# Optimization experiments

Hardware: AMD Instinct MI355X
Metric: run time of the kernel (lower is better)

Reference implementation:

```python
import jax, jax.numpy as jnp
import numpy as np


def _chamfer_min_sqdist(a, b):
    # a: [N,3], b: [M,3] -> for each point in a, min squared distance to b. [N]
    # ||a||^2 + ||b||^2 - 2 a.b^T ; clamp tiny negatives from cancellation.
    a2 = jnp.sum(a * a, axis=-1)            # [N]
    b2 = jnp.sum(b * b, axis=-1)            # [M]
    cross = a @ b.T                          # [N,M] GEMM, K=3
    d = a2[:, None] + b2[None, :] - 2.0 * cross
    return jnp.maximum(jnp.min(d, axis=1), 0.0)


def setup_inputs() -> dict:
    key = jax.random.key(0)
    k1, k2 = jax.random.split(key)
    N = 16384
    state_x = jax.random.normal(k1, (N, 3), dtype=jnp.float32)
    target = jax.random.normal(k2, (N, 3), dtype=jnp.float32)
    return {"state_x": state_x, "target": target}


def reference(state_x, target):
    # dist1: target -> nearest in state_x ; dist2: state_x -> nearest in target
    dist1 = _chamfer_min_sqdist(target, state_x)   # [N]
    dist2 = _chamfer_min_sqdist(state_x, target)   # [N]
    loss = (jnp.mean(jnp.sqrt(dist1)) + jnp.mean(jnp.sqrt(dist2))) * 0.5
    return loss * 10.0
```

## Files before the change

kernel.cpp:

```cpp
#include <hip/hip_runtime.h>
#include <math.h>


typedef __attribute__((ext_vector_type(8)))  short bf16x8;
typedef __attribute__((ext_vector_type(16))) float f32x16;

#define S_SLICES 8

__device__ __forceinline__ unsigned enc_f32(float f) {
    int b = __float_as_int(f);
    return (b >= 0) ? ((unsigned)b | 0x80000000u) : ~(unsigned)b;
}
__device__ __forceinline__ float dec_f32(unsigned k) {
    int b = (k & 0x80000000u) ? (int)(k & 0x7FFFFFFFu) : ~(int)k;
    return __int_as_float(b);
}

__device__ __forceinline__ unsigned short f2bf(float v) {
    unsigned u = __float_as_uint(v);
    u += 0x7FFFu + ((u >> 16) & 1u);
    return (unsigned short)(u >> 16);
}
__device__ __forceinline__ float bf2f(unsigned short b) {
    unsigned u = ((unsigned)b) << 16;
    return __uint_as_float(u);
}
__device__ __forceinline__ unsigned pk2(unsigned short lo, unsigned short hi) {
    return (unsigned)lo | ((unsigned)hi << 16);
}

__global__ __launch_bounds__(256) void chamfer_prep(
    const float* __restrict__ state_x, const float* __restrict__ target,
    uint4* __restrict__ AfragS, uint4* __restrict__ AfragT,
    uint4* __restrict__ BfragS, uint4* __restrict__ BfragT,
    unsigned* __restrict__ mins_u, float* __restrict__ out, int N)
{
    const int p = blockIdx.x * 256 + threadIdx.x;
    const float* src = (p < N) ? state_x : target;
    const int i = (p < N) ? p : p - N;

    const float x = src[3*i+0], y = src[3*i+1], z = src[3*i+2];
    const float n2 = fmaf(x, x, fmaf(y, y, z * z));

    const unsigned short hx = f2bf(x), hy = f2bf(y), hz = f2bf(z);
    const unsigned short lx = f2bf(x - bf2f(hx));
    const unsigned short ly = f2bf(y - bf2f(hy));
    const unsigned short lz = f2bf(z - bf2f(hz));
    const unsigned short mhx = f2bf(-2.0f*x), mhy = f2bf(-2.0f*y), mhz = f2bf(-2.0f*z);
    const unsigned short mlx = f2bf(-2.0f*x - bf2f(mhx));
    const unsigned short mly = f2bf(-2.0f*y - bf2f(mhy));
    const unsigned short mlz = f2bf(-2.0f*z - bf2f(mhz));
    const unsigned short hn = f2bf(n2);
    const unsigned short ln = f2bf(n2 - bf2f(hn));
    const unsigned short ONE = 0x3F80;

    uint4 A0 = make_uint4(pk2(mhx,mhy), pk2(mhz,mlx), pk2(mly,mlz), pk2(mhx,mhy));
    uint4 A1 = make_uint4(pk2(mhz,mlx), pk2(mly,mlz), pk2(hn,ln),   pk2(ONE,ONE));
    uint4 B0 = make_uint4(pk2(hx,hy), pk2(hz,hx), pk2(hy,hz), pk2(lx,ly));
    uint4 B1 = make_uint4(pk2(lz,lx), pk2(ly,lz), pk2(ONE,ONE), pk2(hn,ln));

    uint4* Aarr = (p < N) ? AfragS : AfragT;
    uint4* Barr = (p < N) ? BfragS : BfragT;
    Aarr[2*i+0] = A0;  Aarr[2*i+1] = A1;
    Barr[2*i+0] = B0;  Barr[2*i+1] = B1;

    mins_u[p] = 0xFFFFFFFFu;
    if (p == 0) *out = 0.0f;
}

__global__ __launch_bounds__(256) void chamfer_main(
    const bf16x8* __restrict__ AfragS, const bf16x8* __restrict__ AfragT,
    const bf16x8* __restrict__ BfragS, const bf16x8* __restrict__ BfragT,
    unsigned* __restrict__ mins_u, int N, int S)
{
    const int tid  = threadIdx.x;
    const int lane = tid & 63;
    const int l31  = lane & 31;
    const int half = lane >> 5;
    const int w    = tid >> 6;

    const int bs = blockIdx.x / S;
    const int s  = blockIdx.x % S;
    const int qrow0 = bs * 128 + w * 32;

    const bf16x8* afr;
    const bf16x8* bfr;
    if (qrow0 < N) { afr = AfragT + (size_t)qrow0 * 2;       bfr = BfragS; }
    else           { afr = AfragS + (size_t)(qrow0 - N) * 2; bfr = BfragT; }

    const bf16x8 av = afr[l31 * 2 + half];

    const int C = N / S;
    const bf16x8* bp = bfr + (size_t)(s * C) * 2;
    const int boff = l31 * 2 + half;

    f32x16 racc;
    #pragma unroll
    for (int i = 0; i < 16; ++i) racc[i] = 3.0e38f;
    f32x16 zc;
    #pragma unroll
    for (int i = 0; i < 16; ++i) zc[i] = 0.0f;

    #pragma unroll 2
    for (int it = 0; it < C / 64; ++it) {
        const bf16x8 b0 = bp[it * 128 + boff];
        const bf16x8 b1 = bp[it * 128 + 64 + boff];
        f32x16 acc0 = __builtin_amdgcn_mfma_f32_32x32x16_bf16(av, b0, zc, 0, 0, 0);
        f32x16 acc1 = __builtin_amdgcn_mfma_f32_32x32x16_bf16(av, b1, zc, 0, 0, 0);
        #pragma unroll
        for (int i = 0; i < 16; ++i)
            racc[i] = fminf(fminf(racc[i], acc0[i]), acc1[i]);
    }

    #pragma unroll
    for (int i = 0; i < 16; ++i) {
        float v = racc[i];
        v = fminf(v, __shfl_xor(v, 16, 64));
        v = fminf(v, __shfl_xor(v,  8, 64));
        v = fminf(v, __shfl_xor(v,  4, 64));
        v = fminf(v, __shfl_xor(v,  2, 64));
        v = fminf(v, __shfl_xor(v,  1, 64));
        racc[i] = v;
    }

    if (l31 == 0) {
        #pragma unroll
        for (int i = 0; i < 16; ++i) {
            const int row = (i & 3) + 8 * (i >> 2) + 4 * half;
            atomicMin(&mins_u[qrow0 + row], enc_f32(racc[i]));
        }
    }
}

__global__ __launch_bounds__(256) void chamfer_finish(
    const unsigned* __restrict__ mins_u, float* __restrict__ out, int N)
{
    const int tid = threadIdx.x;
    const int qi = blockIdx.x * 256 + tid;

    float v = sqrtf(fmaxf(dec_f32(mins_u[qi]), 0.0f));

    for (int off = 32; off > 0; off >>= 1) v += __shfl_down(v, off, 64);
    __shared__ float wsum[4];
    if ((tid & 63) == 0) wsum[tid >> 6] = v;
    __syncthreads();
    if (tid == 0) {
        const float bsum = wsum[0] + wsum[1] + wsum[2] + wsum[3];
        atomicAdd(out, bsum * 5.0f / (float)N);
    }
}

extern "C" void kernel_launch(void* const* d_in, const int* in_sizes, int n_in,
                              void* d_out, int out_size, void* d_ws, size_t ws_size,
                              hipStream_t stream)
{
    const float* state_x = (const float*)d_in[0];
    const float* target  = (const float*)d_in[1];
    float* out = (float*)d_out;

    const int N = in_sizes[0] / 3;
    const int twoN = 2 * N;

    int S = S_SLICES;
    while (S > 1 && (N % (S * 64)) != 0) S >>= 1;

    char* wsb = (char*)d_ws;
    unsigned* mins_u = (unsigned*)wsb;
    uint4* AfragS = (uint4*)(wsb + (size_t)twoN * 4);
    uint4* AfragT = (uint4*)(wsb + (size_t)twoN * 4 + (size_t)N * 32);
    uint4* BfragS = (uint4*)(wsb + (size_t)twoN * 4 + (size_t)N * 64);
    uint4* BfragT = (uint4*)(wsb + (size_t)twoN * 4 + (size_t)N * 96);

    chamfer_prep<<<twoN / 256, 256, 0, stream>>>(
        state_x, target, AfragS, AfragT, BfragS, BfragT, mins_u, out, N);

    const int rowBlocks = twoN / 128;
    chamfer_main<<<rowBlocks * S, 256, 0, stream>>>(
        (const bf16x8*)AfragS, (const bf16x8*)AfragT,
        (const bf16x8*)BfragS, (const bf16x8*)BfragT, mins_u, N, S);

    chamfer_finish<<<twoN / 256, 256, 0, stream>>>(mins_u, out, N);
}
```

Baseline: 91.36 us.

## Stage B slice in LDS and compute two 32-row query tiles per wave

Each block now handles 256 query rows, with each wave computing two 32-row A fragments against the same B fragments. The B slice (1024 points) is staged once into shared memory, replacing per-wave global reads. Slices double to 16 to keep the grid size. This raises MFMA work per B load and reuses B across waves, but the LDS copy is hard-coded to 2048 uint4, which assumes C = N/S = 1024.

```diff
diff --git a/kernel.cpp b/kernel.cpp
--- a/kernel.cpp
+++ b/kernel.cpp
@@ -5,7 +5,7 @@
 typedef __attribute__((ext_vector_type(8)))  short bf16x8;
 typedef __attribute__((ext_vector_type(16))) float f32x16;
 
-#define S_SLICES 8
+#define S_SLICES 16
 
 __device__ __forceinline__ unsigned enc_f32(float f) {
     int b = __float_as_int(f);
@@ -81,53 +81,79 @@
 
     const int bs = blockIdx.x / S;
     const int s  = blockIdx.x % S;
-    const int qrow0 = bs * 128 + w * 32;
+    const int qblk = bs * 256;
 
     const bf16x8* afr;
     const bf16x8* bfr;
-    if (qrow0 < N) { afr = AfragT + (size_t)qrow0 * 2;       bfr = BfragS; }
-    else           { afr = AfragS + (size_t)(qrow0 - N) * 2; bfr = BfragT; }
-
-    const bf16x8 av = afr[l31 * 2 + half];
+    if (qblk < N) { afr = AfragT + (size_t)qblk * 2;       bfr = BfragS; }
+    else          { afr = AfragS + (size_t)(qblk - N) * 2; bfr = BfragT; }
 
     const int C = N / S;
-    const bf16x8* bp = bfr + (size_t)(s * C) * 2;
+
+    __shared__ uint4 ldsB[2048];
+    {
+        const uint4* src = (const uint4*)bfr + (size_t)(s * C) * 2;
+        #pragma unroll
+        for (int j = 0; j < 8; ++j)
+            ldsB[tid + j * 256] = src[tid + j * 256];
+    }
+    __syncthreads();
+    const bf16x8* lb = (const bf16x8*)ldsB;
+
+    const int r0 = w * 64;
+    const bf16x8 av0 = afr[(r0 +      l31) * 2 + half];
+    const bf16x8 av1 = afr[(r0 + 32 + l31) * 2 + half];
+
     const int boff = l31 * 2 + half;
 
-    f32x16 racc;
+    f32x16 racc0, racc1, zc;
     #pragma unroll
-    for (int i = 0; i < 16; ++i) racc[i] = 3.0e38f;
-    f32x16 zc;
-    #pragma unroll
-    for (int i = 0; i < 16; ++i) zc[i] = 0.0f;
+    for (int i = 0; i < 16; ++i) { racc0[i] = 3.0e38f; racc1[i] = 3.0e38f; zc[i] = 0.0f; }
 
     #pragma unroll 2
     for (int it = 0; it < C / 64; ++it) {
-        const bf16x8 b0 = bp[it * 128 + boff];
-        const bf16x8 b1 = bp[it * 128 + 64 + boff];
-        f32x16 acc0 = __builtin_amdgcn_mfma_f32_32x32x16_bf16(av, b0, zc, 0, 0, 0);
-        f32x16 acc1 = __builtin_amdgcn_mfma_f32_32x32x16_bf16(av, b1, zc, 0, 0, 0);
-        #pragma unroll
-        for (int i = 0; i < 16; ++i)
-            racc[i] = fminf(fminf(racc[i], acc0[i]), acc1[i]);
+        const bf16x8 b0 = lb[it * 128 + boff];
+        const bf16x8 b1 = lb[it * 128 + 64 + boff];
+        {
+            f32x16 a0 = __builtin_amdgcn_mfma_f32_32x32x16_bf16(av0, b0, zc, 0, 0, 0);
+            f32x16 a1 = __builtin_amdgcn_mfma_f32_32x32x16_bf16(av0, b1, zc, 0, 0, 0);
+            #pragma unroll
+            for (int i = 0; i < 16; ++i)
+                racc0[i] = fminf(fminf(racc0[i], a0[i]), a1[i]);
+        }
+        {
+            f32x16 a0 = __builtin_amdgcn_mfma_f32_32x32x16_bf16(av1, b0, zc, 0, 0, 0);
+            f32x16 a1 = __builtin_amdgcn_mfma_f32_32x32x16_bf16(av1, b1, zc, 0, 0, 0);
+            #pragma unroll
+            for (int i = 0; i < 16; ++i)
+                racc1[i] = fminf(fminf(racc1[i], a0[i]), a1[i]);
+        }
     }
 
     #pragma unroll
     for (int i = 0; i < 16; ++i) {
-        float v = racc[i];
-        v = fminf(v, __shfl_xor(v, 16, 64));
-        v = fminf(v, __shfl_xor(v,  8, 64));
-        v = fminf(v, __shfl_xor(v,  4, 64));
-        v = fminf(v, __shfl_xor(v,  2, 64));
-        v = fminf(v, __shfl_xor(v,  1, 64));
-        racc[i] = v;
+        float v0 = racc0[i], v1 = racc1[i];
+        v0 = fminf(v0, __shfl_xor(v0, 16, 64));
+        v1 = fminf(v1, __shfl_xor(v1, 16, 64));
+        v0 = fminf(v0, __shfl_xor(v0,  8, 64));
+        v1 = fminf(v1, __shfl_xor(v1,  8, 64));
+        v0 = fminf(v0, __shfl_xor(v0,  4, 64));
+        v1 = fminf(v1, __shfl_xor(v1,  4, 64));
+        v0 = fminf(v0, __shfl_xor(v0,  2, 64));
+        v1 = fminf(v1, __shfl_xor(v1,  2, 64));
+        v0 = fminf(v0, __shfl_xor(v0,  1, 64));
+        v1 = fminf(v1, __shfl_xor(v1,  1, 64));
+        racc0[i] = v0;
+        racc1[i] = v1;
     }
 
     if (l31 == 0) {
+        const int base = qblk + r0;
         #pragma unroll
         for (int i = 0; i < 16; ++i) {
             const int row = (i & 3) + 8 * (i >> 2) + 4 * half;
-            atomicMin(&mins_u[qrow0 + row], enc_f32(racc[i]));
+            atomicMin(&mins_u[base + row],      enc_f32(racc0[i]));
+            atomicMin(&mins_u[base + 32 + row], enc_f32(racc1[i]));
         }
     }
 }
@@ -174,7 +200,7 @@
     chamfer_prep<<<twoN / 256, 256, 0, stream>>>(
         state_x, target, AfragS, AfragT, BfragS, BfragT, mins_u, out, N);
 
-    const int rowBlocks = twoN / 128;
+    const int rowBlocks = twoN / 256;
     chamfer_main<<<rowBlocks * S, 256, 0, stream>>>(
         (const bf16x8*)AfragS, (const bf16x8*)AfragT,
         (const bf16x8*)BfragS, (const bf16x8*)BfragT, mins_u, N, S);
```

Result: slower. 94.61 us (+3.6%).
